# Kernel tuning notes

Measured on AMD Instinct MI355X. Metric: run time of the kernel, lower is better.

The kernel has to match this reference:

```python
import jax, jax.numpy as jnp
import numpy as np

EMBED_DIM = 1024
HEADS = 16
DIM_HEAD = 64  # embed_dim // heads
SCALE = DIM_HEAD ** -0.5


def setup_inputs() -> dict:
    key = jax.random.key(0)
    ks = jax.random.split(key, 6)
    x = jax.random.normal(ks[0], (2, 2048, EMBED_DIM), dtype=jnp.float32)
    # qkv_proj: Linear(embed_dim, 3*embed_dim) with bias
    w_qkv = jax.random.normal(ks[1], (EMBED_DIM, 3 * EMBED_DIM), dtype=jnp.float32) * (EMBED_DIM ** -0.5)
    b_qkv = jax.random.normal(ks[2], (3 * EMBED_DIM,), dtype=jnp.float32) * 0.01
    # out_proj: Linear(embed_dim, embed_dim) with bias
    w_out = jax.random.normal(ks[3], (EMBED_DIM, EMBED_DIM), dtype=jnp.float32) * (EMBED_DIM ** -0.5)
    b_out = jax.random.normal(ks[4], (EMBED_DIM,), dtype=jnp.float32) * 0.01
    return {"x": x, "w_qkv": w_qkv, "b_qkv": b_qkv, "w_out": w_out, "b_out": b_out}


def reference(x, w_qkv, b_qkv, w_out, b_out):
    b, s, d = x.shape
    h, dh = HEADS, d // HEADS
    qkv = x @ w_qkv + b_qkv                       # [b, s, 3d]
    qkv = qkv.reshape(b, s, 3, h, dh)
    qkv = jnp.transpose(qkv, (0, 3, 2, 1, 4))     # [b, h, 3, s, dh]
    q, k, v = qkv[:, :, 0], qkv[:, :, 1], qkv[:, :, 2]
    q = q * SCALE
    attn = jnp.einsum("bhqd,bhkd->bhqk", q, k)    # [b, h, s, s]
    attn = jax.nn.softmax(attn.astype(jnp.float32), axis=-1).astype(attn.dtype)
    # attn_dropout p=0 -> identity
    out = jnp.einsum("bhqk,bhkd->bhqd", attn, v)  # [b, h, s, dh]
    out = jnp.transpose(out, (0, 2, 1, 3)).reshape(b, s, d)
    return out @ w_out + b_out
```

## Files before the change

kernel.cpp:

```cpp
#include <hip/hip_runtime.h>

#define EMBED  1024
#define HEADS  16
#define DHEAD  64
#define SEQ    2048
#define BATCH  2
#define NTOK   4096
#define QSCALE 0.125f

typedef unsigned short u16t;
typedef float f32x4 __attribute__((ext_vector_type(4)));
typedef __bf16 bf16x8 __attribute__((ext_vector_type(8)));
typedef u16t u16x8 __attribute__((ext_vector_type(8)));
typedef u16t u16x4 __attribute__((ext_vector_type(4)));

static __device__ __forceinline__ u16t f2bf(float f) {
    unsigned u = __builtin_bit_cast(unsigned, f);
    return (u16t)((u + 0x7fffu + ((u >> 16) & 1u)) >> 16);
}
static __device__ __forceinline__ bf16x8 asbf(u16x8 v) {
    return __builtin_bit_cast(bf16x8, v);
}
static __device__ __forceinline__ f32x4 mfma16(bf16x8 a, bf16x8 b, f32x4 c) {
    return __builtin_amdgcn_mfma_f32_16x16x32_bf16(a, b, c, 0, 0, 0);
}

__global__ __launch_bounds__(256)
void xcvt(const float* __restrict__ X, u16t* __restrict__ XB)
{
    const size_t i = ((size_t)blockIdx.x * 256 + threadIdx.x) * 8;
    float4 a = *(const float4*)&X[i];
    float4 b = *(const float4*)&X[i + 4];
    u16x8 o;
    o[0] = f2bf(a.x); o[1] = f2bf(a.y); o[2] = f2bf(a.z); o[3] = f2bf(a.w);
    o[4] = f2bf(b.x); o[5] = f2bf(b.y); o[6] = f2bf(b.z); o[7] = f2bf(b.w);
    *(u16x8*)&XB[i] = o;
}

__global__ __launch_bounds__(256)
void wtrans(const float* __restrict__ W, u16t* __restrict__ WT, int K, int N)
{
    __shared__ float L[64][65];
    const int t = threadIdx.x;
    const int k0 = blockIdx.y * 64, n0 = blockIdx.x * 64;
#pragma unroll
    for (int rep = 0; rep < 4; ++rep) {
        const int id = rep * 256 + t;
        const int kk = id >> 4, nc = (id & 15) * 4;
        float4 v = *(const float4*)&W[(size_t)(k0 + kk) * N + n0 + nc];
        L[kk][nc] = v.x; L[kk][nc + 1] = v.y; L[kk][nc + 2] = v.z; L[kk][nc + 3] = v.w;
    }
    __syncthreads();
#pragma unroll
    for (int rep = 0; rep < 2; ++rep) {
        const int id = rep * 256 + t;
        const int n = id >> 3, kc = (id & 7) * 8;
        u16x8 o;
#pragma unroll
        for (int i = 0; i < 8; ++i) o[i] = f2bf(L[kc + i][n]);
        *(u16x8*)&WT[(size_t)(n0 + n) * K + k0 + kc] = o;
    }
}

__global__ __launch_bounds__(256)
void vtrans(const u16t* __restrict__ V, u16t* __restrict__ Vt)
{
    __shared__ u16t L[64][65];
    const int t = threadIdx.x;
    const int bh = blockIdx.y;
    const int s0 = blockIdx.x * 64;
    const u16t* src = V + ((size_t)bh * SEQ + s0) * DHEAD;
#pragma unroll
    for (int rep = 0; rep < 2; ++rep) {
        const int id = rep * 256 + t;
        const int s = id >> 3, dc = (id & 7) * 8;
        u16x8 v = *(const u16x8*)&src[(size_t)s * DHEAD + dc];
#pragma unroll
        for (int i = 0; i < 8; ++i) L[s][dc + i] = v[i];
    }
    __syncthreads();
    u16t* dstb = Vt + (size_t)bh * DHEAD * SEQ + s0;
#pragma unroll
    for (int rep = 0; rep < 2; ++rep) {
        const int id = rep * 256 + t;
        const int d = id >> 3, sc = (id & 7) * 8;
        u16x8 o;
#pragma unroll
        for (int i = 0; i < 8; ++i) o[i] = L[sc + i][d];
        *(u16x8*)&dstb[(size_t)d * SEQ + sc] = o;
    }
}

__global__ __launch_bounds__(256)
void gemm_bf16(const u16t* __restrict__ A, const u16t* __restrict__ BT,
               const float* __restrict__ bias, int N, int mode,
               float* __restrict__ C0, u16t* __restrict__ Qo,
               u16t* __restrict__ Ko, u16t* __restrict__ Vo)
{
    __shared__ __align__(16) u16t Al[128][72];
    __shared__ __align__(16) u16t Bl[128][72];
    const int t = threadIdx.x;
    const int lane = t & 63;
    const int g = lane >> 4, l15 = lane & 15;
    const int w = t >> 6, wr = w >> 1, wc = w & 1;
    const int m0 = blockIdx.y * 128, n0 = blockIdx.x * 128;
    const int srow = t >> 3, scol = (t & 7) * 8;

    f32x4 acc[4][4] = {};

    for (int k0 = 0; k0 < EMBED; k0 += 64) {
        __syncthreads();
#pragma unroll
        for (int rep = 0; rep < 4; ++rep) {
            const int row = rep * 32 + srow;
            *(u16x8*)&Al[row][scol] =
                *(const u16x8*)&A[(size_t)(m0 + row) * EMBED + k0 + scol];
            *(u16x8*)&Bl[row][scol] =
                *(const u16x8*)&BT[(size_t)(n0 + row) * EMBED + k0 + scol];
        }
        __syncthreads();
#pragma unroll
        for (int kk = 0; kk < 2; ++kk) {
            bf16x8 av[4], bv[4];
#pragma unroll
            for (int i = 0; i < 4; ++i) {
                av[i] = asbf(*(const u16x8*)&Al[wr * 64 + i * 16 + l15][kk * 32 + g * 8]);
                bv[i] = asbf(*(const u16x8*)&Bl[wc * 64 + i * 16 + l15][kk * 32 + g * 8]);
            }
#pragma unroll
            for (int i = 0; i < 4; ++i)
#pragma unroll
                for (int j = 0; j < 4; ++j)
                    acc[i][j] = mfma16(av[i], bv[j], acc[i][j]);
        }
    }

#pragma unroll
    for (int i = 0; i < 4; ++i)
#pragma unroll
        for (int j = 0; j < 4; ++j)
#pragma unroll
            for (int r = 0; r < 4; ++r) {
                const int row = m0 + wr * 64 + i * 16 + g * 4 + r;
                const int col = n0 + wc * 64 + j * 16 + l15;
                float v = acc[i][j][r] + bias[col];
                if (mode == 0) {
                    C0[(size_t)row * N + col] = v;
                } else {
                    const int tt = col >> 10, c1 = col & 1023;
                    const int h = c1 >> 6, d = c1 & 63;
                    const int b = row >> 11, s = row & 2047;
                    if (tt == 0) v *= QSCALE;
                    u16t* dst = (tt == 0) ? Qo : (tt == 1 ? Ko : Vo);
                    dst[(((size_t)b * HEADS + h) * SEQ + s) * DHEAD + d] = f2bf(v);
                }
            }
}

__global__ __launch_bounds__(256)
void attn_mfma(const u16t* __restrict__ Q, const u16t* __restrict__ K,
               const u16t* __restrict__ Vt, u16t* __restrict__ AO)
{
    __shared__ __align__(16) u16t Kl[64][72];
    __shared__ __align__(16) u16t Vl[64][72];
    const int t = threadIdx.x;
    const int lane = t & 63, wq = t >> 6;
    const int g = lane >> 4, l15 = lane & 15;
    const int bh = blockIdx.y;
    const int q0 = blockIdx.x * 64;
    const int b = bh >> 4, h = bh & 15;

    const u16t* qrow = Q + ((size_t)bh * SEQ + q0 + wq * 16 + l15) * DHEAD;
    bf16x8 qf[2];
    qf[0] = asbf(*(const u16x8*)&qrow[g * 8]);
    qf[1] = asbf(*(const u16x8*)&qrow[32 + g * 8]);

    const int srow = t >> 3, scol = (t & 7) * 8;
    const u16t* Kb = K + (size_t)bh * SEQ * DHEAD;
    const u16t* Vb = Vt + (size_t)bh * DHEAD * SEQ;

    f32x4 accO[4] = {};
    float mrun = -1e30f, lrun = 0.f;

    for (int kv0 = 0; kv0 < SEQ; kv0 += 64) {
        __syncthreads();
#pragma unroll
        for (int rep = 0; rep < 2; ++rep) {
            const int r = rep * 32 + srow;
            *(u16x8*)&Kl[r][scol] = *(const u16x8*)&Kb[(size_t)(kv0 + r) * DHEAD + scol];
            *(u16x8*)&Vl[r][scol] = *(const u16x8*)&Vb[(size_t)r * SEQ + kv0 + scol];
        }
        __syncthreads();

        f32x4 s4[4] = {};
#pragma unroll
        for (int kk = 0; kk < 2; ++kk)
#pragma unroll
            for (int mf = 0; mf < 4; ++mf) {
                bf16x8 a = asbf(*(const u16x8*)&Kl[mf * 16 + l15][kk * 32 + g * 8]);
                s4[mf] = mfma16(a, qf[kk], s4[mf]);
            }

        float mt = s4[0][0];
#pragma unroll
        for (int mf = 0; mf < 4; ++mf)
#pragma unroll
            for (int r = 0; r < 4; ++r) mt = fmaxf(mt, s4[mf][r]);
        mt = fmaxf(mt, __shfl_xor(mt, 16));
        mt = fmaxf(mt, __shfl_xor(mt, 32));
        const float mnew = fmaxf(mrun, mt);
        const float alpha = __expf(mrun - mnew);
        mrun = mnew;

        float p[4][4]; float rs = 0.f;
#pragma unroll
        for (int mf = 0; mf < 4; ++mf)
#pragma unroll
            for (int r = 0; r < 4; ++r) { p[mf][r] = __expf(s4[mf][r] - mnew); rs += p[mf][r]; }
        rs += __shfl_xor(rs, 16);
        rs += __shfl_xor(rs, 32);
        lrun = lrun * alpha + rs;

        u16x8 pu[2];
#pragma unroll
        for (int kk = 0; kk < 2; ++kk)
#pragma unroll
            for (int j = 0; j < 8; ++j)
                pu[kk][j] = f2bf(p[kk * 2 + (j >> 2)][j & 3]);

        float al[4];
#pragma unroll
        for (int r = 0; r < 4; ++r) al[r] = __shfl(alpha, g * 4 + r);
#pragma unroll
        for (int nf = 0; nf < 4; ++nf)
#pragma unroll
            for (int r = 0; r < 4; ++r) accO[nf][r] *= al[r];

#pragma unroll
        for (int kk = 0; kk < 2; ++kk)
#pragma unroll
            for (int nf = 0; nf < 4; ++nf) {
                const u16t* vr = &Vl[nf * 16 + l15][0];
                u16x4 lo = *(const u16x4*)&vr[kk * 32 + g * 4];
                u16x4 hi = *(const u16x4*)&vr[kk * 32 + 16 + g * 4];
                u16x8 bb = __builtin_shufflevector(lo, hi, 0, 1, 2, 3, 4, 5, 6, 7);
                accO[nf] = mfma16(asbf(pu[kk]), asbf(bb), accO[nf]);
            }
    }

    const float inv = 1.f / lrun;
    float iv[4];
#pragma unroll
    for (int r = 0; r < 4; ++r) iv[r] = __shfl(inv, g * 4 + r);
#pragma unroll
    for (int nf = 0; nf < 4; ++nf)
#pragma unroll
        for (int r = 0; r < 4; ++r) {
            const int s = q0 + wq * 16 + g * 4 + r;
            AO[((size_t)b * SEQ + s) * EMBED + h * DHEAD + nf * 16 + l15] =
                f2bf(accO[nf][r] * iv[r]);
        }
}

extern "C" void kernel_launch(void* const* d_in, const int* in_sizes, int n_in,
                              void* d_out, int out_size, void* d_ws, size_t ws_size,
                              hipStream_t stream)
{
    const float* x     = (const float*)d_in[0];
    const float* w_qkv = (const float*)d_in[1];
    const float* b_qkv = (const float*)d_in[2];
    const float* w_out = (const float*)d_in[3];
    const float* b_out = (const float*)d_in[4];

    u16t* xb  = (u16t*)d_ws;
    u16t* wqt = xb  + (size_t)NTOK * EMBED;
    u16t* wot = wqt + (size_t)3072 * 1024;
    u16t* Qb  = wot + (size_t)1024 * 1024;
    u16t* Kb  = Qb  + (size_t)NTOK * EMBED;
    u16t* Vb  = Kb  + (size_t)NTOK * EMBED;
    u16t* Vtb = Vb  + (size_t)NTOK * EMBED;
    u16t* AOb = Vtb + (size_t)NTOK * EMBED;

    xcvt<<<2048, 256, 0, stream>>>(x, xb);
    wtrans<<<dim3(48, 16), 256, 0, stream>>>(w_qkv, wqt, 1024, 3072);
    wtrans<<<dim3(16, 16), 256, 0, stream>>>(w_out, wot, 1024, 1024);

    gemm_bf16<<<dim3(24, 32), 256, 0, stream>>>(xb, wqt, b_qkv, 3072, 1,
                                                nullptr, Qb, Kb, Vb);
    vtrans<<<dim3(32, 32), 256, 0, stream>>>(Vb, Vtb);
    attn_mfma<<<dim3(32, 32), 256, 0, stream>>>(Qb, Kb, Vtb, AOb);
    gemm_bf16<<<dim3(8, 32), 256, 0, stream>>>(AOb, wot, b_out, 1024, 0,
                                               (float*)d_out, nullptr, nullptr, nullptr);
}
```

Measured before the change: 240.9 us.

## Use direct global-to-LDS loads, exp2 softmax with deferred rescale, packed bf16 convert

The GEMM now stages tiles with global_load_lds 16-byte loads straight into unpadded LDS, removing the register round trip. That also drops the row padding, which may add LDS bank conflicts. Attention folds log2(e) into the Q scale so it can use the raw exp2 instruction, and it skips the running-max update and accumulator rescale whenever no lane's new max exceeds the running max by more than a threshold. The probabilities are packed to bf16 with the hardware v_cvt_pk_bf16_f32 instruction instead of manual rounding.

```diff
diff --git a/kernel.cpp b/kernel.cpp
--- a/kernel.cpp
+++ b/kernel.cpp
@@ -6,13 +6,15 @@
 #define SEQ    2048
 #define BATCH  2
 #define NTOK   4096
-#define QSCALE 0.125f
+#define QS2    (0.125f * 1.44269504089f)
+#define DEFER_THR 8.0f
 
 typedef unsigned short u16t;
 typedef float f32x4 __attribute__((ext_vector_type(4)));
 typedef __bf16 bf16x8 __attribute__((ext_vector_type(8)));
 typedef u16t u16x8 __attribute__((ext_vector_type(8)));
 typedef u16t u16x4 __attribute__((ext_vector_type(4)));
+typedef unsigned u32x4 __attribute__((ext_vector_type(4)));
 
 static __device__ __forceinline__ u16t f2bf(float f) {
     unsigned u = __builtin_bit_cast(unsigned, f);
@@ -23,6 +25,17 @@
 }
 static __device__ __forceinline__ f32x4 mfma16(bf16x8 a, bf16x8 b, f32x4 c) {
     return __builtin_amdgcn_mfma_f32_16x16x32_bf16(a, b, c, 0, 0, 0);
+}
+static __device__ __forceinline__ unsigned cvtpk(float lo, float hi) {
+    unsigned r;
+    asm("v_cvt_pk_bf16_f32 %0, %1, %2" : "=v"(r) : "v"(lo), "v"(hi));
+    return r;
+}
+
+typedef const __attribute__((address_space(1))) void* as1cv;
+typedef __attribute__((address_space(3))) void* as3v;
+static __device__ __forceinline__ void ldsload16(const void* g, void* l) {
+    __builtin_amdgcn_global_load_lds((as1cv)g, (as3v)l, 16, 0, 0);
 }
 
 __global__ __launch_bounds__(256)
@@ -97,26 +110,27 @@
                float* __restrict__ C0, u16t* __restrict__ Qo,
                u16t* __restrict__ Ko, u16t* __restrict__ Vo)
 {
-    __shared__ __align__(16) u16t Al[128][72];
-    __shared__ __align__(16) u16t Bl[128][72];
+    __shared__ __align__(16) u16t Al[128 * 64];
+    __shared__ __align__(16) u16t Bl[128 * 64];
     const int t = threadIdx.x;
     const int lane = t & 63;
     const int g = lane >> 4, l15 = lane & 15;
     const int w = t >> 6, wr = w >> 1, wc = w & 1;
     const int m0 = blockIdx.y * 128, n0 = blockIdx.x * 128;
-    const int srow = t >> 3, scol = (t & 7) * 8;
+
+    const int srow = w * 32;
+    const int lrow = lane >> 3;
+    const int lcol = (lane & 7) * 8;
 
     f32x4 acc[4][4] = {};
 
     for (int k0 = 0; k0 < EMBED; k0 += 64) {
         __syncthreads();
 #pragma unroll
-        for (int rep = 0; rep < 4; ++rep) {
-            const int row = rep * 32 + srow;
-            *(u16x8*)&Al[row][scol] =
-                *(const u16x8*)&A[(size_t)(m0 + row) * EMBED + k0 + scol];
-            *(u16x8*)&Bl[row][scol] =
-                *(const u16x8*)&BT[(size_t)(n0 + row) * EMBED + k0 + scol];
+        for (int r = 0; r < 4; ++r) {
+            const int row = srow + r * 8;
+            ldsload16(&A [(size_t)(m0 + row + lrow) * EMBED + k0 + lcol], &Al[row * 64]);
+            ldsload16(&BT[(size_t)(n0 + row + lrow) * EMBED + k0 + lcol], &Bl[row * 64]);
         }
         __syncthreads();
 #pragma unroll
@@ -124,8 +138,8 @@
             bf16x8 av[4], bv[4];
 #pragma unroll
             for (int i = 0; i < 4; ++i) {
-                av[i] = asbf(*(const u16x8*)&Al[wr * 64 + i * 16 + l15][kk * 32 + g * 8]);
-                bv[i] = asbf(*(const u16x8*)&Bl[wc * 64 + i * 16 + l15][kk * 32 + g * 8]);
+                av[i] = asbf(*(const u16x8*)&Al[(wr * 64 + i * 16 + l15) * 64 + kk * 32 + g * 8]);
+                bv[i] = asbf(*(const u16x8*)&Bl[(wc * 64 + i * 16 + l15) * 64 + kk * 32 + g * 8]);
             }
 #pragma unroll
             for (int i = 0; i < 4; ++i)
@@ -150,7 +164,7 @@
                     const int tt = col >> 10, c1 = col & 1023;
                     const int h = c1 >> 6, d = c1 & 63;
                     const int b = row >> 11, s = row & 2047;
-                    if (tt == 0) v *= QSCALE;
+                    if (tt == 0) v *= QS2;
                     u16t* dst = (tt == 0) ? Qo : (tt == 1 ? Ko : Vo);
                     dst[(((size_t)b * HEADS + h) * SEQ + s) * DHEAD + d] = f2bf(v);
                 }
@@ -208,33 +222,47 @@
             for (int r = 0; r < 4; ++r) mt = fmaxf(mt, s4[mf][r]);
         mt = fmaxf(mt, __shfl_xor(mt, 16));
         mt = fmaxf(mt, __shfl_xor(mt, 32));
-        const float mnew = fmaxf(mrun, mt);
-        const float alpha = __expf(mrun - mnew);
-        mrun = mnew;
+
+        const bool skip = __all(mt - mrun <= DEFER_THR) != 0;
+        const float mnew = skip ? mrun : fmaxf(mrun, mt);
 
         float p[4][4]; float rs = 0.f;
 #pragma unroll
         for (int mf = 0; mf < 4; ++mf)
 #pragma unroll
-            for (int r = 0; r < 4; ++r) { p[mf][r] = __expf(s4[mf][r] - mnew); rs += p[mf][r]; }
+            for (int r = 0; r < 4; ++r) {
+                p[mf][r] = __builtin_amdgcn_exp2f(s4[mf][r] - mnew);
+                rs += p[mf][r];
+            }
         rs += __shfl_xor(rs, 16);
         rs += __shfl_xor(rs, 32);
-        lrun = lrun * alpha + rs;
+
+        if (skip) {
+            lrun += rs;
+        } else {
+            const float alpha = __builtin_amdgcn_exp2f(mrun - mnew);
+            lrun = lrun * alpha + rs;
+            mrun = mnew;
+            float al[4];
+#pragma unroll
+            for (int r = 0; r < 4; ++r) al[r] = __shfl(alpha, g * 4 + r);
+#pragma unroll
+            for (int nf = 0; nf < 4; ++nf)
+#pragma unroll
+                for (int r = 0; r < 4; ++r) accO[nf][r] *= al[r];
+        }
 
         u16x8 pu[2];
 #pragma unroll
-        for (int kk = 0; kk < 2; ++kk)
-#pragma unroll
-            for (int j = 0; j < 8; ++j)
-                pu[kk][j] = f2bf(p[kk * 2 + (j >> 2)][j & 3]);
-
-        float al[4];
-#pragma unroll
-        for (int r = 0; r < 4; ++r) al[r] = __shfl(alpha, g * 4 + r);
-#pragma unroll
-        for (int nf = 0; nf < 4; ++nf)
-#pragma unroll
-            for (int r = 0; r < 4; ++r) accO[nf][r] *= al[r];
+        for (int kk = 0; kk < 2; ++kk) {
+            const int a = kk * 2;
+            u32x4 pw;
+            pw[0] = cvtpk(p[a][0], p[a][1]);
+            pw[1] = cvtpk(p[a][2], p[a][3]);
+            pw[2] = cvtpk(p[a + 1][0], p[a + 1][1]);
+            pw[3] = cvtpk(p[a + 1][2], p[a + 1][3]);
+            pu[kk] = __builtin_bit_cast(u16x8, pw);
+        }
 
 #pragma unroll
         for (int kk = 0; kk < 2; ++kk)
```

Measured after the change: 242.8 us. About the same (+0.8%).
